# Kernel optimization log

Hardware: AMD Instinct MI355X
Metric: run time of the kernel (lower is better)

The kernel has to match this reference:

```python
import jax, jax.numpy as jnp
from jax import lax
import numpy as np

B, T, D_IN, H = 8, 2048, 256, 512


def setup_inputs() -> dict:
    key = jax.random.key(0)
    ks = jax.random.split(key, 9)
    s_in = 1.0 / np.sqrt(D_IN)
    s_h = 1.0 / np.sqrt(H)
    return {
        "x": jax.random.normal(ks[0], (B, T, D_IN), jnp.float32),
        "w0_w": jax.random.normal(ks[1], (4 * H, D_IN), jnp.float32) * s_in,
        "w0_b": jax.random.normal(ks[2], (4 * H,), jnp.float32) * s_in,
        "u0_w": jax.random.normal(ks[3], (4 * H, H), jnp.float32) * s_h,
        "u0_b": jax.random.normal(ks[4], (4 * H,), jnp.float32) * s_h,
        "w1_w": jax.random.normal(ks[5], (4 * H, H), jnp.float32) * s_h,
        "w1_b": jax.random.normal(ks[6], (4 * H,), jnp.float32) * s_h,
        "u1_w": jax.random.normal(ks[7], (4 * H, H), jnp.float32) * s_h,
        "u1_b": jax.random.normal(ks[8], (4 * H,), jnp.float32) * s_h,
    }


def _lstm_layer(x, wW, wb, uW, ub):
    # x: [B, T, D]; precompute input projection once (as the torch code does)
    wx = jnp.einsum("btd,gd->btg", x, wW) + wb  # [B, T, 4H]
    b = x.shape[0]
    h0 = jnp.zeros((b, H), x.dtype)
    c0 = jnp.zeros((b, H), x.dtype)

    def step(carry, wx_t):
        h, c = carry
        gates = wx_t + h @ uW.T + ub  # [B, 4H]
        it, ft, gt, ot = jnp.split(gates, 4, axis=-1)
        it = jax.nn.sigmoid(it)
        ft = jax.nn.sigmoid(ft)
        gt = jnp.tanh(gt)
        ot = jax.nn.sigmoid(ot)
        c = ft * c + it * gt
        # custom nonlinearity 'relu' on cell state; eval-mode drop mask = 1.0
        h = ot * jax.nn.relu(c)
        return (h, c), (h, c)

    _, (hs, cs) = lax.scan(step, (h0, c0), wx.transpose(1, 0, 2))
    return hs.transpose(1, 0, 2), cs.transpose(1, 0, 2)  # [B, T, H]


def reference(x, w0_w, w0_b, u0_w, u0_b, w1_w, w1_b, u1_w, u1_b):
    h1, c1 = _lstm_layer(x, w0_w, w0_b, u0_w, u0_b)
    h2, c2 = _lstm_layer(h1, w1_w, w1_b, u1_w, u1_b)
    # stacked last hidden/cell states per layer: [num_layers, B, H]
    hh = jnp.stack([h1[:, -1, :], h2[:, -1, :]], axis=0)
    cc = jnp.stack([c1[:, -1, :], c2[:, -1, :]], axis=0)
    return h2, hh, cc
```

## Files before the change

### kernel.cpp

```cpp
#include <hip/hip_runtime.h>
#include <hip/hip_bf16.h>
#include <stdint.h>


typedef __hip_bfloat16 bf16;
typedef float  floatx4 __attribute__((ext_vector_type(4)));
typedef short  short8  __attribute__((ext_vector_type(8)));
typedef short  short4v __attribute__((ext_vector_type(4)));
typedef unsigned long long u64;

#define T_STEPS  2048
#define SENT64   0xFFFFFFFFFFFFFFFFull
#define HH_OFF   8388608
#define CC_OFF   8396800
#define STR0     1056
#define STR1     2080
#define BUFSZ    16640
#define N_BLK    512
#define N_TICK   32
#define GUARD_MAX (1 << 18)

static __device__ __forceinline__ float bs2f(short s) {
  union { unsigned int u; float f; } c;
  c.u = ((unsigned int)(unsigned short)s) << 16;
  return c.f;
}
static __device__ __forceinline__ short f2bs(float x) {
  union { bf16 h; short s; } u;
  u.h = __float2bfloat16(x);
  return u.s;
}
static __device__ __forceinline__ float sigm(float x) {
  x = fminf(fmaxf(x, -30.f), 30.f);
  return 1.f / (1.f + __expf(-x));
}
static __device__ __forceinline__ float tanhf_(float x) {
  x = fminf(fmaxf(x, -15.f), 15.f);
  float e = __expf(2.f * x);
  return (e - 1.f) / (e + 1.f);
}
static __device__ __forceinline__ floatx4 mfma_bf16(short8 a, short8 b, floatx4 c) {
  return __builtin_amdgcn_mfma_f32_16x16x32_bf16(a, b, c, 0, 0, 0);
}
static __device__ __forceinline__ u64 cload(const u64* p) {
  return __hip_atomic_load(p, __ATOMIC_RELAXED, __HIP_MEMORY_SCOPE_AGENT);
}
static __device__ __forceinline__ void cstore(u64* p, u64 v) {
  __hip_atomic_store(p, v, __ATOMIC_RELAXED, __HIP_MEMORY_SCOPE_AGENT);
}

static __device__ __forceinline__ void poll_fetch_q(const u64* paylT, int wv,
                                                    int lane, char* buf,
                                                    int stride, int colOff) {
  const u64* p = paylT + wv * 256 + lane * 4;
  u64 q0, q1, q2, q3;
  int guard = 0;
  for (;;) {
    q0 = cload(p);     q1 = cload(p + 1);
    q2 = cload(p + 2); q3 = cload(p + 3);
    int ok = (q0 != SENT64) & (q1 != SENT64) & (q2 != SENT64) & (q3 != SENT64);
    if (__all(ok)) break;
    if (++guard > GUARD_MAX) break;
  }
  char* base = buf + colOff + wv * 256 + (lane >> 2) * 16;
  const int r0 = (lane & 3) * 2;
  *reinterpret_cast<u64*>(base + (long)r0 * stride)           = q0;
  *reinterpret_cast<u64*>(base + (long)r0 * stride + 8)       = q1;
  *reinterpret_cast<u64*>(base + (long)(r0 + 1) * stride)     = q2;
  *reinterpret_cast<u64*>(base + (long)(r0 + 1) * stride + 8) = q3;
}
static __device__ __forceinline__ void poll_fetch_q2(const u64* p0T, const u64* p1T,
                                                     int wv, int lane, char* buf) {
  const u64* p0 = p0T + wv * 256 + lane * 4;
  const u64* p1 = p1T + wv * 256 + lane * 4;
  u64 a0, a1, a2, a3, b0, b1, b2, b3;
  int guard = 0;
  for (;;) {
    a0 = cload(p0);     a1 = cload(p0 + 1);
    a2 = cload(p0 + 2); a3 = cload(p0 + 3);
    b0 = cload(p1);     b1 = cload(p1 + 1);
    b2 = cload(p1 + 2); b3 = cload(p1 + 3);
    int ok = (a0 != SENT64) & (a1 != SENT64) & (a2 != SENT64) & (a3 != SENT64) &
             (b0 != SENT64) & (b1 != SENT64) & (b2 != SENT64) & (b3 != SENT64);
    if (__all(ok)) break;
    if (++guard > GUARD_MAX) break;
  }
  char* base0 = buf + wv * 256 + (lane >> 2) * 16;
  const int r0 = (lane & 3) * 2;
  *reinterpret_cast<u64*>(base0 + (long)r0 * STR1)           = a0;
  *reinterpret_cast<u64*>(base0 + (long)r0 * STR1 + 8)       = a1;
  *reinterpret_cast<u64*>(base0 + (long)(r0 + 1) * STR1)     = a2;
  *reinterpret_cast<u64*>(base0 + (long)(r0 + 1) * STR1 + 8) = a3;
  char* base1 = base0 + 1024;
  *reinterpret_cast<u64*>(base1 + (long)r0 * STR1)           = b0;
  *reinterpret_cast<u64*>(base1 + (long)r0 * STR1 + 8)       = b1;
  *reinterpret_cast<u64*>(base1 + (long)(r0 + 1) * STR1)     = b2;
  *reinterpret_cast<u64*>(base1 + (long)(r0 + 1) * STR1 + 8) = b3;
}

__global__ __launch_bounds__(256)
void cvt_f32_bf16(const float* __restrict__ src, bf16* __restrict__ dst, int n) {
  int i = (blockIdx.x * 256 + threadIdx.x) * 4;
  if (i < n) {
    floatx4 v = *reinterpret_cast<const floatx4*>(src + i);
    short4v o;
    #pragma unroll
    for (int r = 0; r < 4; ++r) o[r] = f2bs(v[r]);
    *reinterpret_cast<short4v*>(dst + i) = o;
  }
}

__global__ __launch_bounds__(256)
void gemm_proj(const float* __restrict__ Af, const bf16* __restrict__ W,
               const float* __restrict__ bias, bf16* __restrict__ out,
               int K, int strideB, int strideT)
{
  const int lane  = threadIdx.x & 63;
  const int wave  = threadIdx.x >> 6;
  const int q     = lane >> 4;
  const int c     = lane & 15;
  const int mtile = blockIdx.x;
  const int nbase = blockIdx.y * 256 + wave * 64;
  const int m     = mtile * 16 + c;

  const long abase = (long)(m & 7) * strideB + (long)(m >> 3) * strideT + q * 8;
  const bf16* W0 = W + (long)(nbase +  0 + c) * K + q * 8;
  const bf16* W1 = W + (long)(nbase + 16 + c) * K + q * 8;
  const bf16* W2 = W + (long)(nbase + 32 + c) * K + q * 8;
  const bf16* W3 = W + (long)(nbase + 48 + c) * K + q * 8;

  floatx4 acc0 = {0.f, 0.f, 0.f, 0.f};
  floatx4 acc1 = acc0, acc2 = acc0, acc3 = acc0;
  const int nk = K >> 5;
  for (int kt = 0; kt < nk; ++kt) {
    short8 a;
    floatx4 lo = *reinterpret_cast<const floatx4*>(Af + abase + kt * 32);
    floatx4 hi = *reinterpret_cast<const floatx4*>(Af + abase + kt * 32 + 4);
    #pragma unroll
    for (int r = 0; r < 4; ++r) { a[r] = f2bs(lo[r]); a[4 + r] = f2bs(hi[r]); }
    short8 b0 = *reinterpret_cast<const short8*>(W0 + kt * 32);
    short8 b1 = *reinterpret_cast<const short8*>(W1 + kt * 32);
    short8 b2 = *reinterpret_cast<const short8*>(W2 + kt * 32);
    short8 b3 = *reinterpret_cast<const short8*>(W3 + kt * 32);
    acc0 = mfma_bf16(a, b0, acc0);
    acc1 = mfma_bf16(a, b1, acc1);
    acc2 = mfma_bf16(a, b2, acc2);
    acc3 = mfma_bf16(a, b3, acc3);
  }

  floatx4 accs[4] = {acc0, acc1, acc2, acc3};
  #pragma unroll
  for (int nt = 0; nt < 4; ++nt) {
    const int n = nbase + nt * 16 + c;
    const float bv = bias[n];
    #pragma unroll
    for (int r = 0; r < 4; ++r) {
      const int mrow = mtile * 16 + q * 4 + r;
      out[(long)mrow * 2048 + n] = __float2bfloat16(accs[nt][r] + bv);
    }
  }
}

__global__ __launch_bounds__(256)
void lstm_fused(const bf16* __restrict__ wx, const bf16* __restrict__ Ub0,
                const bf16* __restrict__ Wb1, const bf16* __restrict__ Ub1,
                const float* __restrict__ ub0, const float* __restrict__ w1b,
                const float* __restrict__ u1b, float* __restrict__ out,
                u64* __restrict__ payl0, u64* __restrict__ payl1,
                unsigned int* __restrict__ done, unsigned int* __restrict__ claim)
{
  __shared__ char lds[2 * BUFSZ];
  __shared__ int s_ticket;
  if (threadIdx.x == 0) {
    int xcd = 0;
    asm volatile("s_getreg_b32 %0, hwreg(HW_REG_XCC_ID)" : "=s"(xcd));
    int tk = -1;
    if ((xcd & 7) == 0) {
      unsigned int t = __hip_atomic_fetch_add(claim, 1u, __ATOMIC_RELAXED,
                                              __HIP_MEMORY_SCOPE_AGENT);
      if (t < (unsigned)N_TICK) tk = (int)t;
    }
    s_ticket = tk;
  }
  __syncthreads();
  const int ticket = s_ticket;

  if (ticket < 0) {
    float a0 = (float)threadIdx.x, a1 = a0 + 1.f, a2 = a0 + 2.f, a3 = a0 + 3.f;
    float a4 = a0 + 4.f, a5 = a0 + 5.f, a6 = a0 + 6.f, a7 = a0 + 7.f;
    const float xm = 1.0000001f, ya = 1e-7f;
    int g = 0;
    for (;;) {
      #pragma unroll
      for (int it = 0; it < 64; ++it) {
        asm volatile("v_fmac_f32 %0, %1, %2" : "+v"(a0) : "v"(xm), "v"(ya));
        asm volatile("v_fmac_f32 %0, %1, %2" : "+v"(a1) : "v"(xm), "v"(ya));
        asm volatile("v_fmac_f32 %0, %1, %2" : "+v"(a2) : "v"(xm), "v"(ya));
        asm volatile("v_fmac_f32 %0, %1, %2" : "+v"(a3) : "v"(xm), "v"(ya));
        asm volatile("v_fmac_f32 %0, %1, %2" : "+v"(a4) : "v"(xm), "v"(ya));
        asm volatile("v_fmac_f32 %0, %1, %2" : "+v"(a5) : "v"(xm), "v"(ya));
        asm volatile("v_fmac_f32 %0, %1, %2" : "+v"(a6) : "v"(xm), "v"(ya));
        asm volatile("v_fmac_f32 %0, %1, %2" : "+v"(a7) : "v"(xm), "v"(ya));
      }
      ++g;
      if ((g & 31) == 0) {
        if (__hip_atomic_load(done, __ATOMIC_RELAXED,
                              __HIP_MEMORY_SCOPE_AGENT) >= (unsigned)N_TICK) break;
      }
      if (g > (1 << 16)) break;
    }
    return;
  }

  asm volatile("s_setprio 3" ::: "memory");
  const int wv    = threadIdx.x >> 6;
  const int lane  = threadIdx.x & 63;
  const int q     = lane >> 4;
  const int b     = lane & 15;
  const int layer = ticket >> 4;
  const int grp   = ticket & 15;
  const int blk   = grp * 4 + wv;
  const int jbase = blk * 8;
  const int jj    = jbase + (q & 1) * 4;

  const int row0 = (b < 8) ? (jbase + b) : (512 + jbase + b - 8);
  const int row1 = (b < 8) ? (1024 + jbase + b) : (1536 + jbase + b - 8);

  float* hh = out + ((layer == 0) ? HH_OFF : HH_OFF + 4096);
  float* cc = out + ((layer == 0) ? CC_OFF : CC_OFF + 4096);

  if (layer == 0) {
    short8 a0[16], a1[16];
    {
      const bf16* U0p = Ub0 + (long)row0 * 512 + q * 8;
      const bf16* U1p = Ub0 + (long)row1 * 512 + q * 8;
      #pragma unroll
      for (int kt = 0; kt < 16; ++kt) {
        a0[kt] = *reinterpret_cast<const short8*>(U0p + kt * 32);
        a1[kt] = *reinterpret_cast<const short8*>(U1p + kt * 32);
      }
    }
    float ubi[4], ubf[4], ubg[4], ubo[4];
    #pragma unroll
    for (int r = 0; r < 4; ++r) {
      ubi[r] = ub0[        jj + r];
      ubf[r] = ub0[ 512 + jj + r];
      ubg[r] = ub0[1024 + jj + r];
      ubo[r] = ub0[1536 + jj + r];
    }
    float cst[4] = {0.f, 0.f, 0.f, 0.f};

    const bf16* wxbase = wx + (b & 7) * 2048 + jj;
    short4v vi = *reinterpret_cast<const short4v*>(wxbase);
    short4v vf = *reinterpret_cast<const short4v*>(wxbase + 512);
    short4v vg = *reinterpret_cast<const short4v*>(wxbase + 1024);
    short4v vo = *reinterpret_cast<const short4v*>(wxbase + 1536);

    for (int t = 0; t < T_STEPS; ++t) {
      float wxi[4], wxf[4], wxg[4], wxo[4];
      #pragma unroll
      for (int r = 0; r < 4; ++r) {
        wxi[r] = bs2f(vi[r]); wxf[r] = bs2f(vf[r]);
        wxg[r] = bs2f(vg[r]); wxo[r] = bs2f(vo[r]);
      }
      if (t + 1 < T_STEPS) {
        const bf16* wn = wxbase + (long)(t + 1) * 16384;
        vi = *reinterpret_cast<const short4v*>(wn);
        vf = *reinterpret_cast<const short4v*>(wn + 512);
        vg = *reinterpret_cast<const short4v*>(wn + 1024);
        vo = *reinterpret_cast<const short4v*>(wn + 1536);
      }

      char* buf = lds + (t & 1) * BUFSZ;
      floatx4 acc0 = {0.f, 0.f, 0.f, 0.f};
      floatx4 acc1 = {0.f, 0.f, 0.f, 0.f};

      if (t > 0)
        poll_fetch_q(payl0 + (long)(t - 1) * 1024, wv, lane, buf, STR0, 0);
      __syncthreads();
      if (t > 0) {
        #pragma unroll
        for (int kt = 0; kt < 16; ++kt) {
          short8 hb = *reinterpret_cast<const short8*>(
              buf + (b & 7) * STR0 + kt * 64 + q * 16);
          acc0 = mfma_bf16(a0[kt], hb, acc0);
          acc1 = mfma_bf16(a1[kt], hb, acc1);
        }
      }

      float fsh[4], osh[4];
      #pragma unroll
      for (int r = 0; r < 4; ++r) {
        fsh[r] = __shfl_xor(acc0[r], 32, 64);
        osh[r] = __shfl_xor(acc1[r], 32, 64);
      }

      if (q < 2 && b < 8) {
        short4v hp4; floatx4 hf4, cf4;
        #pragma unroll
        for (int r = 0; r < 4; ++r) {
          const float pi = acc0[r] + wxi[r] + ubi[r];
          const float pf = fsh[r]  + wxf[r] + ubf[r];
          const float pg = acc1[r] + wxg[r] + ubg[r];
          const float po = osh[r]  + wxo[r] + ubo[r];
          const float it = sigm(pi), ft = sigm(pf);
          const float gt = tanhf_(pg), ot = sigm(po);
          const float cv = ft * cst[r] + it * gt;
          cst[r] = cv;
          const float hv = ot * fmaxf(cv, 0.f);
          hf4[r] = hv; cf4[r] = cv; hp4[r] = f2bs(hv);
        }
        union { short4v v; u64 u; } pk; pk.v = hp4;
        cstore(payl0 + (long)t * 1024 + blk * 16 + (b * 2 + (q & 1)), pk.u);
        if (t == T_STEPS - 1) {
          *reinterpret_cast<floatx4*>(hh + b * 512 + jj) = hf4;
          *reinterpret_cast<floatx4*>(cc + b * 512 + jj) = cf4;
        }
      }
    }
  } else {
    short8 a0[32], a1[32];
    {
      const bf16* W0p = Wb1 + (long)row0 * 512 + q * 8;
      const bf16* W1p = Wb1 + (long)row1 * 512 + q * 8;
      const bf16* U0p = Ub1 + (long)row0 * 512 + q * 8;
      const bf16* U1p = Ub1 + (long)row1 * 512 + q * 8;
      #pragma unroll
      for (int kt = 0; kt < 16; ++kt) {
        a0[kt]      = *reinterpret_cast<const short8*>(W0p + kt * 32);
        a1[kt]      = *reinterpret_cast<const short8*>(W1p + kt * 32);
        a0[16 + kt] = *reinterpret_cast<const short8*>(U0p + kt * 32);
        a1[16 + kt] = *reinterpret_cast<const short8*>(U1p + kt * 32);
      }
    }
    float ubi[4], ubf[4], ubg[4], ubo[4];
    #pragma unroll
    for (int r = 0; r < 4; ++r) {
      ubi[r] = w1b[        jj + r] + u1b[        jj + r];
      ubf[r] = w1b[ 512 + jj + r] + u1b[ 512 + jj + r];
      ubg[r] = w1b[1024 + jj + r] + u1b[1024 + jj + r];
      ubo[r] = w1b[1536 + jj + r] + u1b[1536 + jj + r];
    }
    float cst[4] = {0.f, 0.f, 0.f, 0.f};

    for (int t = 0; t < T_STEPS; ++t) {
      char* buf = lds + (t & 1) * BUFSZ;
      floatx4 acc0 = {0.f, 0.f, 0.f, 0.f};
      floatx4 acc1 = {0.f, 0.f, 0.f, 0.f};

      if (t > 0) {
        poll_fetch_q2(payl0 + (long)t * 1024, payl1 + (long)(t - 1) * 1024,
                      wv, lane, buf);
      } else {
        poll_fetch_q(payl0, wv, lane, buf, STR1, 0);
      }
      __syncthreads();

      #pragma unroll
      for (int kt = 0; kt < 16; ++kt) {
        short8 hb = *reinterpret_cast<const short8*>(
            buf + (b & 7) * STR1 + kt * 64 + q * 16);
        acc0 = mfma_bf16(a0[kt], hb, acc0);
        acc1 = mfma_bf16(a1[kt], hb, acc1);
      }
      if (t > 0) {
        #pragma unroll
        for (int kt = 16; kt < 32; ++kt) {
          short8 hb = *reinterpret_cast<const short8*>(
              buf + (b & 7) * STR1 + kt * 64 + q * 16);
          acc0 = mfma_bf16(a0[kt], hb, acc0);
          acc1 = mfma_bf16(a1[kt], hb, acc1);
        }
      }

      float fsh[4], osh[4];
      #pragma unroll
      for (int r = 0; r < 4; ++r) {
        fsh[r] = __shfl_xor(acc0[r], 32, 64);
        osh[r] = __shfl_xor(acc1[r], 32, 64);
      }

      if (q < 2 && b < 8) {
        short4v hp4; floatx4 hf4, cf4;
        #pragma unroll
        for (int r = 0; r < 4; ++r) {
          const float pi = acc0[r] + ubi[r];
          const float pf = fsh[r]  + ubf[r];
          const float pg = acc1[r] + ubg[r];
          const float po = osh[r]  + ubo[r];
          const float it = sigm(pi), ft = sigm(pf);
          const float gt = tanhf_(pg), ot = sigm(po);
          const float cv = ft * cst[r] + it * gt;
          cst[r] = cv;
          const float hv = ot * fmaxf(cv, 0.f);
          hf4[r] = hv; cf4[r] = cv; hp4[r] = f2bs(hv);
        }
        union { short4v v; u64 u; } pk; pk.v = hp4;
        cstore(payl1 + (long)t * 1024 + blk * 16 + (b * 2 + (q & 1)), pk.u);
        *reinterpret_cast<floatx4*>(out + (long)b * 1048576 + (long)t * 512 + jj) = hf4;
        if (t == T_STEPS - 1) {
          *reinterpret_cast<floatx4*>(hh + b * 512 + jj) = hf4;
          *reinterpret_cast<floatx4*>(cc + b * 512 + jj) = cf4;
        }
      }
    }
  }

  __syncthreads();
  if (threadIdx.x == 0) {
    __hip_atomic_fetch_add(done, 1u, __ATOMIC_RELAXED, __HIP_MEMORY_SCOPE_AGENT);
  }
}

extern "C" void kernel_launch(void* const* d_in, const int* in_sizes, int n_in,
                              void* d_out, int out_size, void* d_ws, size_t ws_size,
                              hipStream_t stream) {
  (void)in_sizes; (void)n_in; (void)out_size; (void)ws_size;
  const float* x   = (const float*)d_in[0];
  const float* w0w = (const float*)d_in[1];
  const float* w0b = (const float*)d_in[2];
  const float* u0w = (const float*)d_in[3];
  const float* u0b = (const float*)d_in[4];
  const float* w1w = (const float*)d_in[5];
  const float* w1b = (const float*)d_in[6];
  const float* u1w = (const float*)d_in[7];
  const float* u1b = (const float*)d_in[8];
  float* out = (float*)d_out;

  char* ws = (char*)d_ws;
  u64*  payl0 = (u64*)ws;
  u64*  payl1 = (u64*)(ws + (size_t)16777216);
  bf16* Wb0 = (bf16*)(ws + (size_t)33554432);
  bf16* Ub0 = (bf16*)(ws + (size_t)34603008);
  bf16* Wb1 = (bf16*)(ws + (size_t)36700160);
  bf16* Ub1 = (bf16*)(ws + (size_t)38797312);
  bf16* wx  = (bf16*)(ws + (size_t)40894464);
  unsigned int* done = (unsigned int*)(ws + (size_t)115343360);

  hipMemsetAsync(ws, 0xFF, (size_t)33554432, stream);
  hipMemsetAsync(done, 0, 64, stream);

  cvt_f32_bf16<<<512,  256, 0, stream>>>(w0w, Wb0, 524288);
  cvt_f32_bf16<<<1024, 256, 0, stream>>>(u0w, Ub0, 1048576);
  cvt_f32_bf16<<<1024, 256, 0, stream>>>(w1w, Wb1, 1048576);
  cvt_f32_bf16<<<1024, 256, 0, stream>>>(u1w, Ub1, 1048576);

  dim3 gg(1024, 8, 1);
  gemm_proj<<<gg, 256, 0, stream>>>(x, Wb0, w0b, wx, 256, 2048 * 256, 256);

  lstm_fused<<<N_BLK, 256, 0, stream>>>(wx, Ub0, Wb1, Ub1, u0b, w1b, u1b,
                                        out, payl0, payl1, done, done + 1);
}
```

Baseline: 7.097 ms.

## Split layer-1 W and U matmuls across paired waves with LDS reduction

Layer 1 now gets 32 workgroups instead of 16, raising the total to 48. Each hidden block is handled by a pair of waves: one wave multiplies the input h1 by W and the other multiplies the recurrent h2 by U. The second wave hands its partial sums to the first through an LDS scratch area, and the first wave then applies the gate nonlinearities. This halves the per-wave serial MFMA chain and register footprint on the critical recurrent path. The cost is an extra __syncthreads per step and more workgroups that must stay co-resident for the spin-wait protocol.

```diff
diff --git a/kernel.cpp b/kernel.cpp
--- a/kernel.cpp
+++ b/kernel.cpp
@@ -17,7 +17,7 @@
 #define STR1     2080
 #define BUFSZ    16640
 #define N_BLK    512
-#define N_TICK   32
+#define N_TICK   48
 #define GUARD_MAX (1 << 18)
 
 static __device__ __forceinline__ float bs2f(short s) {
@@ -169,7 +169,7 @@
                 u64* __restrict__ payl0, u64* __restrict__ payl1,
                 unsigned int* __restrict__ done, unsigned int* __restrict__ claim)
 {
-  __shared__ char lds[2 * BUFSZ];
+  __shared__ char lds[2 * BUFSZ + 4096];
   __shared__ int s_ticket;
   if (threadIdx.x == 0) {
     int xcd = 0;
@@ -217,9 +217,9 @@
   const int lane  = threadIdx.x & 63;
   const int q     = lane >> 4;
   const int b     = lane & 15;
-  const int layer = ticket >> 4;
-  const int grp   = ticket & 15;
-  const int blk   = grp * 4 + wv;
+  const int layer = (ticket < 16) ? 0 : 1;
+  const int blk   = (layer == 0) ? (ticket * 4 + wv)
+                                 : ((ticket - 16) * 2 + (wv >> 1));
   const int jbase = blk * 8;
   const int jj    = jbase + (q & 1) * 4;
 
@@ -319,18 +319,17 @@
       }
     }
   } else {
-    short8 a0[32], a1[32];
+    const int role = wv & 1;
+    char* pairScr = lds + 2 * BUFSZ + (wv >> 1) * 2048;
+    short8 a0[16], a1[16];
     {
-      const bf16* W0p = Wb1 + (long)row0 * 512 + q * 8;
-      const bf16* W1p = Wb1 + (long)row1 * 512 + q * 8;
-      const bf16* U0p = Ub1 + (long)row0 * 512 + q * 8;
-      const bf16* U1p = Ub1 + (long)row1 * 512 + q * 8;
+      const bf16* Wsrc = (role == 0) ? Wb1 : Ub1;
+      const bf16* B0p = Wsrc + (long)row0 * 512 + q * 8;
+      const bf16* B1p = Wsrc + (long)row1 * 512 + q * 8;
       #pragma unroll
       for (int kt = 0; kt < 16; ++kt) {
-        a0[kt]      = *reinterpret_cast<const short8*>(W0p + kt * 32);
-        a1[kt]      = *reinterpret_cast<const short8*>(W1p + kt * 32);
-        a0[16 + kt] = *reinterpret_cast<const short8*>(U0p + kt * 32);
-        a1[16 + kt] = *reinterpret_cast<const short8*>(U1p + kt * 32);
+        a0[kt] = *reinterpret_cast<const short8*>(B0p + kt * 32);
+        a1[kt] = *reinterpret_cast<const short8*>(B1p + kt * 32);
       }
     }
     float ubi[4], ubf[4], ubg[4], ubo[4];
@@ -356,51 +355,65 @@
       }
       __syncthreads();
 
-      #pragma unroll
-      for (int kt = 0; kt < 16; ++kt) {
-        short8 hb = *reinterpret_cast<const short8*>(
-            buf + (b & 7) * STR1 + kt * 64 + q * 16);
-        acc0 = mfma_bf16(a0[kt], hb, acc0);
-        acc1 = mfma_bf16(a1[kt], hb, acc1);
-      }
-      if (t > 0) {
-        #pragma unroll
-        for (int kt = 16; kt < 32; ++kt) {
+      if (role == 0) {
+        #pragma unroll
+        for (int kt = 0; kt < 16; ++kt) {
           short8 hb = *reinterpret_cast<const short8*>(
               buf + (b & 7) * STR1 + kt * 64 + q * 16);
           acc0 = mfma_bf16(a0[kt], hb, acc0);
           acc1 = mfma_bf16(a1[kt], hb, acc1);
         }
-      }
-
-      float fsh[4], osh[4];
-      #pragma unroll
-      for (int r = 0; r < 4; ++r) {
-        fsh[r] = __shfl_xor(acc0[r], 32, 64);
-        osh[r] = __shfl_xor(acc1[r], 32, 64);
-      }
-
-      if (q < 2 && b < 8) {
-        short4v hp4; floatx4 hf4, cf4;
+      } else if (t > 0) {
+        #pragma unroll
+        for (int kt = 0; kt < 16; ++kt) {
+          short8 hb = *reinterpret_cast<const short8*>(
+              buf + (b & 7) * STR1 + 1024 + kt * 64 + q * 16);
+          acc0 = mfma_bf16(a0[kt], hb, acc0);
+          acc1 = mfma_bf16(a1[kt], hb, acc1);
+        }
+      }
+
+      if (role == 1) {
+        *reinterpret_cast<floatx4*>(pairScr + lane * 16)        = acc0;
+        *reinterpret_cast<floatx4*>(pairScr + 1024 + lane * 16) = acc1;
+      }
+      __syncthreads();
+
+      if (role == 0) {
+        floatx4 p0 = *reinterpret_cast<const floatx4*>(pairScr + lane * 16);
+        floatx4 p1 = *reinterpret_cast<const floatx4*>(pairScr + 1024 + lane * 16);
+        #pragma unroll
+        for (int r = 0; r < 4; ++r) { acc0[r] += p0[r]; acc1[r] += p1[r]; }
+
+        float fsh[4], osh[4];
         #pragma unroll
         for (int r = 0; r < 4; ++r) {
-          const float pi = acc0[r] + ubi[r];
-          const float pf = fsh[r]  + ubf[r];
-          const float pg = acc1[r] + ubg[r];
-          const float po = osh[r]  + ubo[r];
-          const float it = sigm(pi), ft = sigm(pf);
-          const float gt = tanhf_(pg), ot = sigm(po);
-          const float cv = ft * cst[r] + it * gt;
-          cst[r] = cv;
-          const float hv = ot * fmaxf(cv, 0.f);
-          hf4[r] = hv; cf4[r] = cv; hp4[r] = f2bs(hv);
-        }
-        union { short4v v; u64 u; } pk; pk.v = hp4;
-        cstore(payl1 + (long)t * 1024 + blk * 16 + (b * 2 + (q & 1)), pk.u);
-        *reinterpret_cast<floatx4*>(out + (long)b * 1048576 + (long)t * 512 + jj) = hf4;
-        if (t == T_STEPS - 1) {
-          *reinterpret_cast<floatx4*>(hh + b * 512 + jj) = hf4;
-          *reinterpret_cast<floatx4*>(cc + b * 512 + jj) = cf4;
+          fsh[r] = __shfl_xor(acc0[r], 32, 64);
+          osh[r] = __shfl_xor(acc1[r], 32, 64);
+        }
+
+        if (q < 2 && b < 8) {
+          short4v hp4; floatx4 hf4, cf4;
+          #pragma unroll
+          for (int r = 0; r < 4; ++r) {
+            const float pi = acc0[r] + ubi[r];
+            const float pf = fsh[r]  + ubf[r];
+            const float pg = acc1[r] + ubg[r];
+            const float po = osh[r]  + ubo[r];
+            const float it = sigm(pi), ft = sigm(pf);
+            const float gt = tanhf_(pg), ot = sigm(po);
+            const float cv = ft * cst[r] + it * gt;
+            cst[r] = cv;
+            const float hv = ot * fmaxf(cv, 0.f);
+            hf4[r] = hv; cf4[r] = cv; hp4[r] = f2bs(hv);
+          }
+          union { short4v v; u64 u; } pk; pk.v = hp4;
+          cstore(payl1 + (long)t * 1024 + blk * 16 + (b * 2 + (q & 1)), pk.u);
+          *reinterpret_cast<floatx4*>(out + (long)b * 1048576 + (long)t * 512 + jj) = hf4;
+          if (t == T_STEPS - 1) {
+            *reinterpret_cast<floatx4*>(hh + b * 512 + jj) = hf4;
+            *reinterpret_cast<floatx4*>(cc + b * 512 + jj) = cf4;
+          }
         }
       }
     }
```

Measured after the change: 9.027 ms. 1.27x slower.
